# Optimization experiments

Hardware: AMD Instinct MI355X
Metric: run time of the kernel (lower is better)

Reference implementation:

```python
import jax, jax.numpy as jnp
import numpy as np

E = 512        # emb_size
H = 2 * E      # LSTM units
B = 512        # beam/query batch (batched Python-loop states)
K = 32         # padded candidates per state
T = 8          # max_path_length
N_ENT = 50000
N_REL = 5000


def setup_inputs() -> dict:
    key = jax.random.key(0)
    ks = jax.random.split(key, 12)
    f32 = jnp.float32
    ent_emb = jax.random.normal(ks[0], (N_ENT, E), f32) * 0.05
    rel_emb = jax.random.normal(ks[1], (N_REL, E), f32) * 0.05
    relation = jax.random.normal(ks[2], (B, E), f32) * 0.05
    Wx = jax.random.normal(ks[3], (H, 4 * H), f32) * 0.02
    Wh = jax.random.normal(ks[4], (H, 4 * H), f32) * 0.02
    b = jnp.zeros((4 * H,), f32)
    W1 = jax.random.normal(ks[5], (4 * E, 3 * E), f32) * 0.02
    b1 = jnp.zeros((3 * E,), f32)
    W2 = jax.random.normal(ks[6], (3 * E, 2 * E), f32) * 0.02
    b2 = jnp.zeros((2 * E,), f32)
    current_ids = jax.random.randint(ks[7], (T, B), 0, N_ENT)
    prev_rel_ids = jax.random.randint(ks[8], (T, B), 0, N_REL)
    cand_rel_ids = jax.random.randint(ks[9], (T, B, K), 0, N_REL)
    cand_ent_ids = jax.random.randint(ks[10], (T, B, K), 0, N_ENT)
    return {
        "ent_emb": ent_emb, "rel_emb": rel_emb, "relation": relation,
        "Wx": Wx, "Wh": Wh, "b": b,
        "W1": W1, "b1": b1, "W2": W2, "b2": b2,
        "current_ids": current_ids, "prev_rel_ids": prev_rel_ids,
        "cand_rel_ids": cand_rel_ids, "cand_ent_ids": cand_ent_ids,
    }


def reference(ent_emb, rel_emb, relation, Wx, Wh, b, W1, b1, W2, b2,
              current_ids, prev_rel_ids, cand_rel_ids, cand_ent_ids):
    Bh = relation.shape[0]
    units = Wh.shape[0]
    h0 = jnp.zeros((Bh, units), ent_emb.dtype)
    c0 = jnp.zeros((Bh, units), ent_emb.dtype)

    def step(carry, xs):
        h, c = carry
        cur, prl, crel, cent = xs
        # LSTMCell input: concat(prev relation vec, current entity vec)  [B, 2E]
        x = jnp.concatenate([rel_emb[prl], ent_emb[cur]], axis=-1)
        z = x @ Wx + h @ Wh + b                      # [B, 4H], keras gate order i,f,g,o
        i_, f_, g_, o_ = jnp.split(z, 4, axis=-1)
        c = jax.nn.sigmoid(f_) * c + jax.nn.sigmoid(i_) * jnp.tanh(g_)
        h = jax.nn.sigmoid(o_) * jnp.tanh(c)
        # posterior MLP on concat(ent, history, relation)  [B, 4E] -> [B, 2E]
        feat = jax.nn.relu(jnp.concatenate([ent_emb[cur], h, relation], axis=-1) @ W1 + b1)
        feat = jax.nn.relu(feat @ W2 + b2)
        # candidate embeddings: concat(rel vec, to-entity vec)  [B, K, 2E]
        cand = jnp.concatenate([rel_emb[crel], ent_emb[cent]], axis=-1)
        probs = jax.nn.softmax(jnp.einsum('bkd,bd->bk', cand, feat), axis=-1)
        return (h, c), probs

    _, probs = jax.lax.scan(step, (h0, c0),
                            (current_ids, prev_rel_ids, cand_rel_ids, cand_ent_ids))
    return probs  # [T, B, K]
```

## Files before the change

### kernel.cpp

```cpp
#include <hip/hip_runtime.h>
#include <stdint.h>

typedef __attribute__((ext_vector_type(4))) float f32x4;
typedef __attribute__((ext_vector_type(8))) __bf16 bf16x8;
typedef __attribute__((ext_vector_type(8))) unsigned short u16x8;
typedef __attribute__((ext_vector_type(4))) unsigned short u16x4;

__device__ __forceinline__ float b2f(unsigned short u) {
  unsigned int x = ((unsigned int)u) << 16;
  float f; __builtin_memcpy(&f, &x, 4); return f;
}
__device__ __forceinline__ unsigned short f2b(float f) {
  unsigned int x; __builtin_memcpy(&x, &f, 4);
  x += 0x7fffu + ((x >> 16) & 1u);
  return (unsigned short)(x >> 16);
}
__device__ __forceinline__ float sigmoidf(float x) {
  return 1.f / (1.f + __expf(-x));
}
__device__ __forceinline__ float tanh_fast(float x) {
  return 1.f - 2.f / (1.f + __expf(2.f * x));
}

__global__ __launch_bounds__(256) void conv_f2b(
    const float* __restrict__ in, unsigned short* __restrict__ out) {
  const int i = blockIdx.x * 256 + threadIdx.x;
  f32x4 a = *(const f32x4*)(in + (size_t)i * 8);
  f32x4 b = *(const f32x4*)(in + (size_t)i * 8 + 4);
  unsigned short t[8];
#pragma unroll
  for (int j = 0; j < 4; j++) { t[j] = f2b(a[j]); t[4+j] = f2b(b[j]); }
  *(u16x8*)(out + (size_t)i * 8) = *(u16x8*)t;
}

__global__ __launch_bounds__(256) void transpose_f2b(
    const float* __restrict__ in, unsigned short* __restrict__ out,
    int R, int C) {
  __shared__ unsigned short tile[64][72];
  const int r0 = blockIdx.y * 64, c0 = blockIdx.x * 64;
  const int tid = threadIdx.x;
  const int r = tid >> 3;
  const int c8 = (tid & 7) * 8;
#pragma unroll
  for (int i = 0; i < 2; i++) {
    const float* src = in + (size_t)(r0 + r + 32*i) * C + c0 + c8;
    f32x4 a = *(const f32x4*)src;
    f32x4 b = *(const f32x4*)(src + 4);
    unsigned short tmp[8];
#pragma unroll
    for (int j = 0; j < 4; j++) { tmp[j] = f2b(a[j]); tmp[4+j] = f2b(b[j]); }
    *(u16x8*)(&tile[r + 32*i][c8]) = *(u16x8*)tmp;
  }
  __syncthreads();
#pragma unroll
  for (int i = 0; i < 2; i++) {
    const int ro = r + 32*i;
    unsigned short tmp[8];
#pragma unroll
    for (int j = 0; j < 8; j++) tmp[j] = tile[c8 + j][ro];
    *(u16x8*)(out + (size_t)(c0 + ro) * R + r0 + c8) = *(u16x8*)tmp;
  }
}

__global__ void gather_all(const unsigned short* __restrict__ entB,
                           const unsigned short* __restrict__ relB,
                           const unsigned short* __restrict__ relationB,
                           const int* __restrict__ cur, const int* __restrict__ prl,
                           unsigned short* __restrict__ Xall,
                           unsigned short* __restrict__ ERall) {
  const int row = blockIdx.x;
  const int b = row & 511;
  const int tid = threadIdx.x;
  const int ci = cur[row], ri = prl[row];
  const unsigned short* xsrc = (tid < 64) ? (relB + (size_t)ri * 512 + tid * 8)
                                          : (entB + (size_t)ci * 512 + (tid - 64) * 8);
  const unsigned short* esrc = (tid < 64) ? (entB + (size_t)ci * 512 + tid * 8)
                                          : (relationB + (size_t)b * 512 + (tid - 64) * 8);
  *(u16x8*)(Xall + (size_t)row * 1024 + tid * 8) = *(const u16x8*)xsrc;
  *(u16x8*)(ERall + (size_t)row * 1024 + tid * 8) = *(const u16x8*)esrc;
}

template<bool HAS_BIAS, bool DO_RELU, bool PERM_B, bool ASPLIT>
__global__ __launch_bounds__(256) void gemm_bf16(
    const unsigned short* __restrict__ A,
    const unsigned short* __restrict__ A2, int lda,
    const unsigned short* __restrict__ BT, int ldb, int K,
    const float* __restrict__ bias,
    unsigned short* __restrict__ Cout, int ldc) {
  __shared__ unsigned short As[128][72];
  __shared__ unsigned short Bs[128][72];
  const int tid = threadIdx.x;
  const int lane = tid & 63;
  const int w = tid >> 6;
  const int wr = w >> 1, wc = w & 1;
  const int m0 = blockIdx.y * 128, n0 = blockIdx.x * 128;
  f32x4 acc[4][4] = {};
  const int rs = tid >> 3;
  const int cs = (tid & 7) * 8;

  for (int k0 = 0; k0 < K; k0 += 64) {
    const unsigned short* asrc; int ac;
    if (ASPLIT) {
      if (k0 < 512)       { asrc = A;  ac = k0; }
      else if (k0 < 1536) { asrc = A2; ac = k0 - 512; }
      else                { asrc = A;  ac = k0 - 1024; }
    } else { asrc = A; ac = k0; }
#pragma unroll
    for (int i = 0; i < 4; i++)
      *(u16x8*)(&As[rs + 32*i][cs]) =
          *(const u16x8*)(asrc + (size_t)(m0 + rs + 32*i) * lda + ac + cs);
#pragma unroll
    for (int i = 0; i < 4; i++) {
      const int brow = n0 + rs + 32*i;
      const int prow = PERM_B ? (((brow & 3) << 10) + (brow >> 2)) : brow;
      *(u16x8*)(&Bs[rs + 32*i][cs]) =
          *(const u16x8*)(BT + (size_t)prow * ldb + k0 + cs);
    }
    __syncthreads();
#pragma unroll
    for (int ks = 0; ks < 2; ks++) {
      const int kb = ks * 32 + (lane >> 4) * 8;
      bf16x8 af[4], bfr[4];
#pragma unroll
      for (int m = 0; m < 4; m++)
        af[m] = *reinterpret_cast<const bf16x8*>(&As[wr*64 + m*16 + (lane & 15)][kb]);
#pragma unroll
      for (int n = 0; n < 4; n++)
        bfr[n] = *reinterpret_cast<const bf16x8*>(&Bs[wc*64 + n*16 + (lane & 15)][kb]);
#pragma unroll
      for (int m = 0; m < 4; m++)
#pragma unroll
        for (int n = 0; n < 4; n++)
          acc[m][n] = __builtin_amdgcn_mfma_f32_16x16x32_bf16(af[m], bfr[n], acc[m][n], 0, 0, 0);
    }
    __syncthreads();
  }

  const int cn = lane & 15, rb = (lane >> 4) * 4;
#pragma unroll
  for (int m = 0; m < 4; m++) {
#pragma unroll
    for (int n = 0; n < 4; n++) {
      const int gn = n0 + wc*64 + n*16 + cn;
#pragma unroll
      for (int r = 0; r < 4; r++) {
        const int gm = m0 + wr*64 + m*16 + rb + r;
        float v = acc[m][n][r];
        if (HAS_BIAS) v += bias[gn];
        if (DO_RELU)  v = v > 0.f ? v : 0.f;
        Cout[(size_t)gm * ldc + gn] = f2b(v);
      }
    }
  }
}

__global__ __launch_bounds__(512) void zgemm_lstm(
    const unsigned short* __restrict__ A,
    const unsigned short* __restrict__ BT,
    const unsigned short* __restrict__ pre,
    const float* __restrict__ bias,
    unsigned short* __restrict__ Hout,
    float* __restrict__ Cst) {
  __shared__ unsigned short As[2][64][72];
  __shared__ unsigned short Bs[2][128][72];
  __shared__ f32x4 accL[8][256];
  const int tid = threadIdx.x;
  const int lane = tid & 63;
  const int w = tid >> 6;
  const int q = w >> 2;
  const int wq = w & 3;
  const int wr = wq >> 1, wc = wq & 1;
  const int m0 = blockIdx.y * 64, n0 = blockIdx.x * 128;
  f32x4 acc[2][4] = {};
  const int tq = tid & 255;
  const int rs = tq >> 3;
  const int cs = (tq & 7) * 8;

  for (int k0 = 0; k0 < 512; k0 += 64) {
    const int kk = q * 512 + k0;
#pragma unroll
    for (int i = 0; i < 2; i++)
      *(u16x8*)(&As[q][rs + 32*i][cs]) =
          *(const u16x8*)(A + (size_t)(m0 + rs + 32*i) * 1024 + kk + cs);
#pragma unroll
    for (int i = 0; i < 4; i++) {
      const int brow = n0 + rs + 32*i;
      const int prow = ((brow & 3) << 10) + (brow >> 2);
      *(u16x8*)(&Bs[q][rs + 32*i][cs]) =
          *(const u16x8*)(BT + (size_t)prow * 1024 + kk + cs);
    }
    __syncthreads();
#pragma unroll
    for (int ks = 0; ks < 2; ks++) {
      const int kb = ks * 32 + (lane >> 4) * 8;
      bf16x8 af[2], bfr[4];
#pragma unroll
      for (int m = 0; m < 2; m++)
        af[m] = *reinterpret_cast<const bf16x8*>(&As[q][wr*32 + m*16 + (lane & 15)][kb]);
#pragma unroll
      for (int n = 0; n < 4; n++)
        bfr[n] = *reinterpret_cast<const bf16x8*>(&Bs[q][wc*64 + n*16 + (lane & 15)][kb]);
#pragma unroll
      for (int m = 0; m < 2; m++)
#pragma unroll
        for (int n = 0; n < 4; n++)
          acc[m][n] = __builtin_amdgcn_mfma_f32_16x16x32_bf16(af[m], bfr[n], acc[m][n], 0, 0, 0);
    }
    __syncthreads();
  }

  if (q == 1) {
#pragma unroll
    for (int m = 0; m < 2; m++)
#pragma unroll
      for (int n = 0; n < 4; n++)
        accL[m*4 + n][tq] = acc[m][n];
  }
  __syncthreads();
  if (q == 0) {
    const int cn = lane & 15, rb = (lane >> 4) * 4, g = lane & 3;
#pragma unroll
    for (int m = 0; m < 2; m++) {
#pragma unroll
      for (int n = 0; n < 4; n++) {
        const f32x4 s4 = accL[m*4 + n][tq];
        const int gn = n0 + wc*64 + n*16 + cn;
        const int u = gn >> 2;
        const float gb = bias[g * 1024 + u];
        const int row0 = m0 + wr*32 + m*16 + rb;
        const float v0 = acc[m][n][0] + s4[0] + b2f(pre[(size_t)(row0+0) * 4096 + gn]) + gb;
        const float v1 = acc[m][n][1] + s4[1] + b2f(pre[(size_t)(row0+1) * 4096 + gn]) + gb;
        const float v2 = acc[m][n][2] + s4[2] + b2f(pre[(size_t)(row0+2) * 4096 + gn]) + gb;
        const float v3 = acc[m][n][3] + s4[3] + b2f(pre[(size_t)(row0+3) * 4096 + gn]) + gb;
        auto sel = [&](int idx) {
          return idx == 0 ? v0 : idx == 1 ? v1 : idx == 2 ? v2 : v3;
        };
        const float own = sel(g);
        const float r1 = __shfl_xor(sel(g ^ 1), 1);
        const float r2 = __shfl_xor(sel(g ^ 2), 2);
        const float r3 = __shfl_xor(sel(g ^ 3), 3);
        const float zi = g==0 ? own : g==1 ? r1 : g==2 ? r2 : r3;
        const float zf = g==0 ? r1  : g==1 ? own: g==2 ? r3 : r2;
        const float zg_= g==0 ? r2  : g==1 ? r3 : g==2 ? own: r1;
        const float zo = g==0 ? r3  : g==1 ? r2 : g==2 ? r1 : own;
        const size_t hidx = (size_t)(row0 + g) * 1024 + u;
        const float cnew = sigmoidf(zf) * Cst[hidx] + sigmoidf(zi) * tanh_fast(zg_);
        const float h = sigmoidf(zo) * tanh_fast(cnew);
        Cst[hidx] = cnew;
        Hout[hidx] = f2b(h);
      }
    }
  }
}

__global__ void lstm_gate0(const unsigned short* __restrict__ P1_,
                           const float* __restrict__ bias,
                           float* __restrict__ C, unsigned short* __restrict__ H) {
  const int idx = blockIdx.x * 256 + threadIdx.x;
  const int b = idx >> 10, u = idx & 1023;
  u16x4 z4 = *(const u16x4*)(P1_ + (size_t)b * 4096 + 4 * u);
  const float i_ = b2f(z4[0]) + bias[u];
  const float g_ = b2f(z4[2]) + bias[2048 + u];
  const float o_ = b2f(z4[3]) + bias[3072 + u];
  const float c = sigmoidf(i_) * tanh_fast(g_);
  const float h = sigmoidf(o_) * tanh_fast(c);
  C[idx] = c;
  H[idx] = f2b(h);
}

__global__ __launch_bounds__(256) void score_softmax(
    const unsigned short* __restrict__ F2,
    const unsigned short* __restrict__ relB,
    const unsigned short* __restrict__ entB,
    const int* __restrict__ crel, const int* __restrict__ cent,
    float* __restrict__ outp) {
  const int b = blockIdx.x;
  const int tid = threadIdx.x;
  const int lane = tid & 63, w = tid >> 6;
  __shared__ float feat[1024];
  __shared__ float logits[32];
  {
    u16x4 fv = ((const u16x4*)(F2 + (size_t)b * 1024))[tid];
#pragma unroll
    for (int j = 0; j < 4; j++) feat[tid * 4 + j] = b2f(fv[j]);
  }
  __syncthreads();
  for (int k = w; k < 32; k += 4) {
    const int ri = crel[b * 32 + k], ei = cent[b * 32 + k];
    u16x8 rv = *(const u16x8*)(relB + (size_t)ri * 512 + lane * 8);
    u16x8 ev = *(const u16x8*)(entB + (size_t)ei * 512 + lane * 8);
    float sum = 0.f;
#pragma unroll
    for (int j = 0; j < 8; j++) {
      sum += b2f(rv[j]) * feat[lane * 8 + j];
      sum += b2f(ev[j]) * feat[512 + lane * 8 + j];
    }
#pragma unroll
    for (int off = 32; off; off >>= 1) sum += __shfl_down(sum, off, 64);
    if (lane == 0) logits[k] = sum;
  }
  __syncthreads();
  if (tid < 32) {
    const float l = logits[tid];
    float mx = l;
#pragma unroll
    for (int off = 16; off; off >>= 1) mx = fmaxf(mx, __shfl_xor(mx, off, 32));
    const float p = __expf(l - mx);
    float s = p;
#pragma unroll
    for (int off = 16; off; off >>= 1) s += __shfl_xor(s, off, 32);
    outp[(size_t)b * 32 + tid] = p / s;
  }
}

extern "C" void kernel_launch(void* const* d_in, const int* in_sizes, int n_in,
                              void* d_out, int out_size, void* d_ws, size_t ws_size,
                              hipStream_t stream) {
  const float* ent      = (const float*)d_in[0];
  const float* rel      = (const float*)d_in[1];
  const float* relation = (const float*)d_in[2];
  const float* Wx       = (const float*)d_in[3];
  const float* Wh       = (const float*)d_in[4];
  const float* bvec     = (const float*)d_in[5];
  const float* W1       = (const float*)d_in[6];
  const float* b1       = (const float*)d_in[7];
  const float* W2       = (const float*)d_in[8];
  const float* b2       = (const float*)d_in[9];
  const int* cur  = (const int*)d_in[10];
  const int* prl  = (const int*)d_in[11];
  const int* crel = (const int*)d_in[12];
  const int* cent = (const int*)d_in[13];
  float* out = (float*)d_out;
  (void)in_sizes; (void)n_in; (void)out_size; (void)ws_size;

  char* wsp = (char*)d_ws;
  auto alloc = [&](size_t bytes) { char* p = wsp; wsp += (bytes + 255) & ~(size_t)255; return p; };
  unsigned short* entB = (unsigned short*)alloc((size_t)50000 * 512 * 2);
  unsigned short* relB = (unsigned short*)alloc((size_t)5000 * 512 * 2);
  unsigned short* rlnB = (unsigned short*)alloc((size_t)512 * 512 * 2);
  unsigned short* WxT  = (unsigned short*)alloc((size_t)4096 * 1024 * 2);
  unsigned short* WhT  = (unsigned short*)alloc((size_t)4096 * 1024 * 2);
  unsigned short* W1T  = (unsigned short*)alloc((size_t)1536 * 2048 * 2);
  unsigned short* W2T  = (unsigned short*)alloc((size_t)1024 * 1536 * 2);
  unsigned short* Xall = (unsigned short*)alloc((size_t)4096 * 1024 * 2);
  unsigned short* ERall= (unsigned short*)alloc((size_t)4096 * 1024 * 2);
  unsigned short* P1   = (unsigned short*)alloc((size_t)4096 * 4096 * 2);
  unsigned short* Hall = (unsigned short*)alloc((size_t)4096 * 1024 * 2);
  unsigned short* F1   = (unsigned short*)alloc((size_t)4096 * 1536 * 2);
  unsigned short* F2   = (unsigned short*)alloc((size_t)4096 * 1024 * 2);
  float*          C    = (float*)         alloc((size_t)512 * 1024 * 4);

  const dim3 blk(256);
  const size_t HS = (size_t)512 * 1024;

  conv_f2b<<<50000 * 512 / 8 / 256, blk, 0, stream>>>(ent, entB);
  conv_f2b<<<5000 * 512 / 8 / 256, blk, 0, stream>>>(rel, relB);
  conv_f2b<<<512 * 512 / 8 / 256, blk, 0, stream>>>(relation, rlnB);
  transpose_f2b<<<dim3(4096/64, 1024/64), blk, 0, stream>>>(Wx, WxT, 1024, 4096);
  transpose_f2b<<<dim3(4096/64, 1024/64), blk, 0, stream>>>(Wh, WhT, 1024, 4096);
  transpose_f2b<<<dim3(1536/64, 2048/64), blk, 0, stream>>>(W1, W1T, 2048, 1536);
  transpose_f2b<<<dim3(1024/64, 1536/64), blk, 0, stream>>>(W2, W2T, 1536, 1024);
  gather_all<<<4096, 128, 0, stream>>>(entB, relB, rlnB, cur, prl, Xall, ERall);

  gemm_bf16<false,false,true,false><<<dim3(32, 32), blk, 0, stream>>>(
      Xall, nullptr, 1024, WxT, 1024, 1024, nullptr, P1, 4096);

  lstm_gate0<<<2048, 256, 0, stream>>>(P1, bvec, C, Hall);
  for (int t = 1; t < 8; t++) {
    zgemm_lstm<<<dim3(32, 8), dim3(512), 0, stream>>>(
        Hall + (size_t)(t - 1) * HS, WhT,
        P1 + (size_t)t * 512 * 4096, bvec,
        Hall + (size_t)t * HS, C);
  }

  gemm_bf16<true,true,false,true><<<dim3(12, 32), blk, 0, stream>>>(
      ERall, Hall, 1024, W1T, 2048, 2048, b1, F1, 1536);
  gemm_bf16<true,true,false,false><<<dim3(8, 32), blk, 0, stream>>>(
      F1, nullptr, 1536, W2T, 1536, 1536, b2, F2, 1024);
  score_softmax<<<4096, 256, 0, stream>>>(F2, relB, entB, crel, cent, out);
}
```

Baseline: 348.2 us.

## Merge conversion/transpose launches and use direct global-to-LDS loads in GEMMs

The three embedding conversion kernels are merged into one launch, and the four weight transposes into another, which cuts launch overhead and tail effects. The bf16 GEMM gains a mode that stages A and B tiles with global_load_lds (direct global-to-LDS, 16 bytes per lane) instead of going through registers, and all three GEMM calls now use it. To fit that instruction's contiguous layout the LDS row padding drops from 72 to 64, which may bring back bank conflicts on the MFMA fragment reads.

Result: no change. 353.3 us (+1.5%).

```diff
diff --git a/kernel.cpp b/kernel.cpp
--- a/kernel.cpp
+++ b/kernel.cpp
@@ -6,6 +6,9 @@
 typedef __attribute__((ext_vector_type(8))) unsigned short u16x8;
 typedef __attribute__((ext_vector_type(4))) unsigned short u16x4;
 
+typedef const __attribute__((address_space(1))) unsigned int gu32;
+typedef __attribute__((address_space(3))) unsigned int lu32;
+
 __device__ __forceinline__ float b2f(unsigned short u) {
   unsigned int x = ((unsigned int)u) << 16;
   float f; __builtin_memcpy(&f, &x, 4); return f;
@@ -22,22 +25,38 @@
   return 1.f - 2.f / (1.f + __expf(2.f * x));
 }
 
-__global__ __launch_bounds__(256) void conv_f2b(
-    const float* __restrict__ in, unsigned short* __restrict__ out) {
-  const int i = blockIdx.x * 256 + threadIdx.x;
-  f32x4 a = *(const f32x4*)(in + (size_t)i * 8);
-  f32x4 b = *(const f32x4*)(in + (size_t)i * 8 + 4);
+__global__ __launch_bounds__(256) void conv_all(
+    const float* __restrict__ ent, unsigned short* __restrict__ entB,
+    const float* __restrict__ rel, unsigned short* __restrict__ relB,
+    const float* __restrict__ rln, unsigned short* __restrict__ rlnB) {
+  const long long N0 = 50000LL * 512 / 8, N1 = 5000LL * 512 / 8, N2 = 512LL * 512 / 8;
+  long long i = (long long)blockIdx.x * 256 + threadIdx.x;
+  if (i >= N0 + N1 + N2) return;
+  const float* in; unsigned short* out;
+  if (i < N0)            { in = ent; out = entB; }
+  else if (i < N0 + N1)  { in = rel; out = relB; i -= N0; }
+  else                   { in = rln; out = rlnB; i -= N0 + N1; }
+  f32x4 a = *(const f32x4*)(in + i * 8);
+  f32x4 b = *(const f32x4*)(in + i * 8 + 4);
   unsigned short t[8];
 #pragma unroll
   for (int j = 0; j < 4; j++) { t[j] = f2b(a[j]); t[4+j] = f2b(b[j]); }
-  *(u16x8*)(out + (size_t)i * 8) = *(u16x8*)t;
-}
-
-__global__ __launch_bounds__(256) void transpose_f2b(
-    const float* __restrict__ in, unsigned short* __restrict__ out,
-    int R, int C) {
+  *(u16x8*)(out + i * 8) = *(u16x8*)t;
+}
+
+__global__ __launch_bounds__(256) void transpose_all(
+    const float* __restrict__ Wx, unsigned short* __restrict__ WxT,
+    const float* __restrict__ Wh, unsigned short* __restrict__ WhT,
+    const float* __restrict__ W1, unsigned short* __restrict__ W1T,
+    const float* __restrict__ W2, unsigned short* __restrict__ W2T) {
   __shared__ unsigned short tile[64][72];
-  const int r0 = blockIdx.y * 64, c0 = blockIdx.x * 64;
+  int b = blockIdx.x;
+  const float* in; unsigned short* out; int R, C, bx, by;
+  if (b < 1024)      { in = Wx; out = WxT; R = 1024; C = 4096; bx = b & 63; by = b >> 6; }
+  else if (b < 2048) { b -= 1024; in = Wh; out = WhT; R = 1024; C = 4096; bx = b & 63; by = b >> 6; }
+  else if (b < 2816) { b -= 2048; in = W1; out = W1T; R = 2048; C = 1536; bx = b % 24; by = b / 24; }
+  else               { b -= 2816; in = W2; out = W2T; R = 1536; C = 1024; bx = b & 15; by = b >> 4; }
+  const int r0 = by * 64, c0 = bx * 64;
   const int tid = threadIdx.x;
   const int r = tid >> 3;
   const int c8 = (tid & 7) * 8;
@@ -45,10 +64,10 @@
   for (int i = 0; i < 2; i++) {
     const float* src = in + (size_t)(r0 + r + 32*i) * C + c0 + c8;
     f32x4 a = *(const f32x4*)src;
-    f32x4 b = *(const f32x4*)(src + 4);
+    f32x4 bb = *(const f32x4*)(src + 4);
     unsigned short tmp[8];
 #pragma unroll
-    for (int j = 0; j < 4; j++) { tmp[j] = f2b(a[j]); tmp[4+j] = f2b(b[j]); }
+    for (int j = 0; j < 4; j++) { tmp[j] = f2b(a[j]); tmp[4+j] = f2b(bb[j]); }
     *(u16x8*)(&tile[r + 32*i][c8]) = *(u16x8*)tmp;
   }
   __syncthreads();
@@ -80,15 +99,16 @@
   *(u16x8*)(ERall + (size_t)row * 1024 + tid * 8) = *(const u16x8*)esrc;
 }
 
-template<bool HAS_BIAS, bool DO_RELU, bool PERM_B, bool ASPLIT>
+template<bool HAS_BIAS, bool DO_RELU, bool PERM_B, bool ASPLIT, bool GLD>
 __global__ __launch_bounds__(256) void gemm_bf16(
     const unsigned short* __restrict__ A,
     const unsigned short* __restrict__ A2, int lda,
     const unsigned short* __restrict__ BT, int ldb, int K,
     const float* __restrict__ bias,
     unsigned short* __restrict__ Cout, int ldc) {
-  __shared__ unsigned short As[128][72];
-  __shared__ unsigned short Bs[128][72];
+  constexpr int LDP = GLD ? 64 : 72;
+  __shared__ unsigned short As[128][LDP];
+  __shared__ unsigned short Bs[128][LDP];
   const int tid = threadIdx.x;
   const int lane = tid & 63;
   const int w = tid >> 6;
@@ -97,6 +117,8 @@
   f32x4 acc[4][4] = {};
   const int rs = tid >> 3;
   const int cs = (tid & 7) * 8;
+  const int srow = lane >> 3;
+  const int scol = (lane & 7) * 8;
 
   for (int k0 = 0; k0 < K; k0 += 64) {
     const unsigned short* asrc; int ac;
@@ -105,16 +127,32 @@
       else if (k0 < 1536) { asrc = A2; ac = k0 - 512; }
       else                { asrc = A;  ac = k0 - 1024; }
     } else { asrc = A; ac = k0; }
-#pragma unroll
-    for (int i = 0; i < 4; i++)
-      *(u16x8*)(&As[rs + 32*i][cs]) =
-          *(const u16x8*)(asrc + (size_t)(m0 + rs + 32*i) * lda + ac + cs);
-#pragma unroll
-    for (int i = 0; i < 4; i++) {
-      const int brow = n0 + rs + 32*i;
-      const int prow = PERM_B ? (((brow & 3) << 10) + (brow >> 2)) : brow;
-      *(u16x8*)(&Bs[rs + 32*i][cs]) =
-          *(const u16x8*)(BT + (size_t)prow * ldb + k0 + cs);
+    if (GLD) {
+#pragma unroll
+      for (int i = 0; i < 4; i++) {
+        const int c = w * 4 + i;
+        const int row = c * 8 + srow;
+        __builtin_amdgcn_global_load_lds(
+            (gu32*)(asrc + (size_t)(m0 + row) * lda + ac + scol),
+            (lu32*)(&As[0][0] + c * 512), 16, 0, 0);
+        const int brow = n0 + row;
+        const int prow = PERM_B ? (((brow & 3) << 10) + (brow >> 2)) : brow;
+        __builtin_amdgcn_global_load_lds(
+            (gu32*)(BT + (size_t)prow * ldb + k0 + scol),
+            (lu32*)(&Bs[0][0] + c * 512), 16, 0, 0);
+      }
+    } else {
+#pragma unroll
+      for (int i = 0; i < 4; i++)
+        *(u16x8*)(&As[rs + 32*i][cs]) =
+            *(const u16x8*)(asrc + (size_t)(m0 + rs + 32*i) * lda + ac + cs);
+#pragma unroll
+      for (int i = 0; i < 4; i++) {
+        const int brow = n0 + rs + 32*i;
+        const int prow = PERM_B ? (((brow & 3) << 10) + (brow >> 2)) : brow;
+        *(u16x8*)(&Bs[rs + 32*i][cs]) =
+            *(const u16x8*)(BT + (size_t)prow * ldb + k0 + cs);
+      }
     }
     __syncthreads();
 #pragma unroll
@@ -353,16 +391,15 @@
   const dim3 blk(256);
   const size_t HS = (size_t)512 * 1024;
 
-  conv_f2b<<<50000 * 512 / 8 / 256, blk, 0, stream>>>(ent, entB);
-  conv_f2b<<<5000 * 512 / 8 / 256, blk, 0, stream>>>(rel, relB);
-  conv_f2b<<<512 * 512 / 8 / 256, blk, 0, stream>>>(relation, rlnB);
-  transpose_f2b<<<dim3(4096/64, 1024/64), blk, 0, stream>>>(Wx, WxT, 1024, 4096);
-  transpose_f2b<<<dim3(4096/64, 1024/64), blk, 0, stream>>>(Wh, WhT, 1024, 4096);
-  transpose_f2b<<<dim3(1536/64, 2048/64), blk, 0, stream>>>(W1, W1T, 2048, 1536);
-  transpose_f2b<<<dim3(1024/64, 1536/64), blk, 0, stream>>>(W2, W2T, 1536, 1024);
+  {
+    const long long tot = 50000LL*512/8 + 5000LL*512/8 + 512LL*512/8;
+    conv_all<<<(unsigned)((tot + 255) / 256), blk, 0, stream>>>(
+        ent, entB, rel, relB, relation, rlnB);
+  }
+  transpose_all<<<3200, blk, 0, stream>>>(Wx, WxT, Wh, WhT, W1, W1T, W2, W2T);
   gather_all<<<4096, 128, 0, stream>>>(entB, relB, rlnB, cur, prl, Xall, ERall);
 
-  gemm_bf16<false,false,true,false><<<dim3(32, 32), blk, 0, stream>>>(
+  gemm_bf16<false,false,true,false,true><<<dim3(32, 32), blk, 0, stream>>>(
       Xall, nullptr, 1024, WxT, 1024, 1024, nullptr, P1, 4096);
 
   lstm_gate0<<<2048, 256, 0, stream>>>(P1, bvec, C, Hall);
@@ -373,9 +410,9 @@
         Hall + (size_t)t * HS, C);
   }
 
-  gemm_bf16<true,true,false,true><<<dim3(12, 32), blk, 0, stream>>>(
+  gemm_bf16<true,true,false,true,true><<<dim3(12, 32), blk, 0, stream>>>(
       ERall, Hall, 1024, W1T, 2048, 2048, b1, F1, 1536);
-  gemm_bf16<true,true,false,false><<<dim3(8, 32), blk, 0, stream>>>(
+  gemm_bf16<true,true,false,false,true><<<dim3(8, 32), blk, 0, stream>>>(
       F1, nullptr, 1536, W2T, 1536, 1536, b2, F2, 1024);
   score_softmax<<<4096, 256, 0, stream>>>(F2, relB, entB, crel, cent, out);
 }
```
